# Performance work log

Hardware: AMD Instinct MI355X
Metric: run time of the kernel (lower is better)

The kernel has to match this reference:

```python
import jax, jax.numpy as jnp
import numpy as np

NUM_LAYERS = 2
VOCAB = 32000
IN_FEAT = 256          # embedding dim is IN_FEAT-1, +1 for cue scalar
HIDDEN = 256
ATN = 64               # hardcoded atn_feature_size in GraphConvolution
CLASSES = 2
B, N = 8, 2048


def setup_inputs() -> dict:
    key = jax.random.key(0)
    ks = jax.random.split(key, 12)
    x = jax.random.randint(ks[0], (B, N), 0, VOCAB, dtype=jnp.int32)
    cue = jax.random.randint(ks[1], (B, N), 0, 2, dtype=jnp.int32)
    adj = (jax.random.uniform(ks[2], (B, N, N)) < 0.01).astype(jnp.float32)
    s = 1.0 / np.sqrt(HIDDEN)
    emb_table = jax.random.normal(ks[3], (VOCAB, IN_FEAT - 1), jnp.float32) * 0.02
    Wh = jax.random.uniform(ks[4], (IN_FEAT, HIDDEN), jnp.float32, -s, s)
    bh = jax.random.uniform(ks[5], (HIDDEN,), jnp.float32, -s, s)
    Wq = jax.random.uniform(ks[6], (HIDDEN, ATN), jnp.float32, -s, s)
    Wk = jax.random.uniform(ks[7], (HIDDEN, ATN), jnp.float32, -s, s)
    Wv = jax.random.uniform(ks[8], (HIDDEN, HIDDEN), jnp.float32, -s, s)
    gcb = jax.random.uniform(ks[9], (HIDDEN,), jnp.float32, -s, s)
    Wc = jax.random.uniform(ks[10], (HIDDEN, CLASSES), jnp.float32, -s, s)
    bc = jax.random.uniform(ks[11], (CLASSES,), jnp.float32, -s, s)
    return {"x": x, "cue": cue, "adj": adj, "emb_table": emb_table,
            "Wh": Wh, "bh": bh, "Wq": Wq, "Wk": Wk, "Wv": Wv,
            "gcb": gcb, "Wc": Wc, "bc": bc}


def graph_attention_layer(h, adj, Wq, Wk, Wv, gcb):
    # h: [B,N,H]; adj: [B,N,N] binary. Per node i: softmax over neighbors j of
    # (Wk h_j) . (Wq h_i), weighted sum of Wv h_j. Zero-degree nodes get 0 (pre-bias).
    q = jnp.einsum('bnh,ha->bna', h, Wq)        # [B,N,A]
    k = jnp.einsum('bnh,ha->bna', h, Wk)        # [B,N,A]
    v = jnp.einsum('bnh,hg->bng', h, Wv)        # [B,N,H]
    logits = jnp.einsum('bia,bja->bij', q, k)   # [B,N,N]
    mask = adj > 0
    attn = jax.nn.softmax(jnp.where(mask, logits, -1e9), axis=-1)
    out = jnp.einsum('bij,bjh->bih', attn, v)   # [B,N,H]
    has_nbr = jnp.any(mask, axis=-1, keepdims=True)  # [B,N,1]
    return jnp.where(has_nbr, out, 0.0) + gcb


def reference(x, cue, adj, emb_table, Wh, bh, Wq, Wk, Wv, gcb, Wc, bc):
    emb = emb_table[x]                                   # [B,N,IN_FEAT-1]
    feats = jnp.concatenate([emb, cue.astype(jnp.float32)[..., None]], axis=-1)
    h = jax.nn.relu(jnp.einsum('bnf,fh->bnh', feats, Wh) + bh)
    for _ in range(NUM_LAYERS):
        h = jax.nn.sigmoid(graph_attention_layer(h, adj, Wq, Wk, Wv, gcb))
    logits = jnp.einsum('bnh,hc->bnc', h, Wc) + bc
    return jax.nn.softmax(logits, axis=-1)
```

## Files before the change

### kernel.cpp

```cpp
#include <hip/hip_runtime.h>
#include <hip/hip_bf16.h>


#define NB 8
#define NN 2048
#define ROWS (NB * NN)
#define MAXD 64
#define CSR1 6144

typedef float f4 __attribute__((ext_vector_type(4)));
typedef _Float16 hf;
typedef _Float16 hx2 __attribute__((ext_vector_type(2)));
typedef _Float16 hx4 __attribute__((ext_vector_type(4)));
typedef _Float16 hx8 __attribute__((ext_vector_type(8)));
typedef unsigned int u32;
typedef unsigned short u16;
typedef u16 us8 __attribute__((ext_vector_type(8)));

__device__ __forceinline__ float sigmoidf_(float x) { return 1.f / (1.f + __expf(-x)); }
__device__ __forceinline__ hx2 u2h(u32 u) { union { u32 u; hx2 h; } c; c.u = u; return c.h; }
__device__ __forceinline__ float dot2_(hx2 a, hx2 b, float c) {
#if __has_builtin(__builtin_amdgcn_fdot2)
    return __builtin_amdgcn_fdot2(a, b, c, false);
#else
    return c + (float)a.x * (float)b.x + (float)a.y * (float)b.y;
#endif
}
__device__ __forceinline__ u32 permlo_(u32 hi, u32 lo) { return __builtin_amdgcn_perm(hi, lo, 0x05040100u); }
__device__ __forceinline__ u32 permhi_(u32 hi, u32 lo) { return __builtin_amdgcn_perm(hi, lo, 0x07060302u); }

__device__ __forceinline__ void csr_row(const float* __restrict__ adj,
                                        int* __restrict__ deg, int* __restrict__ nbr,
                                        int row, int t, int* cnt) {
    const f4* ar4 = (const f4*)(adj + (size_t)row * NN);
    if (t == 0) *cnt = 0;
    __syncthreads();
    int* nr = nbr + (size_t)row * MAXD;
#pragma unroll
    for (int it = 0; it < 2; ++it) {
        int idx = it * 256 + t;
        f4 vv = __builtin_nontemporal_load(ar4 + idx);
        if (vv.x > 0.f) { int p = atomicAdd(cnt, 1); if (p < MAXD) nr[p] = idx * 4 + 0; }
        if (vv.y > 0.f) { int p = atomicAdd(cnt, 1); if (p < MAXD) nr[p] = idx * 4 + 1; }
        if (vv.z > 0.f) { int p = atomicAdd(cnt, 1); if (p < MAXD) nr[p] = idx * 4 + 2; }
        if (vv.w > 0.f) { int p = atomicAdd(cnt, 1); if (p < MAXD) nr[p] = idx * 4 + 3; }
    }
    __syncthreads();
    if (t == 0) deg[row] = (*cnt < MAXD) ? *cnt : MAXD;
}

__global__ __launch_bounds__(256) void k_front1(
        const int* __restrict__ x, const int* __restrict__ cue,
        const float* __restrict__ adj, const float* __restrict__ emb,
        const float* __restrict__ Wh, const float* __restrict__ bh,
        const float* __restrict__ Wq, const float* __restrict__ Wk,
        const float* __restrict__ Wv,
        hf* __restrict__ hB, hf* __restrict__ Wpt,
        int* __restrict__ deg, int* __restrict__ nbr) {
    __shared__ float As[32 * 64];
    __shared__ float Ws[32 * 128];
    int bid = blockIdx.x;
    int t = threadIdx.x;

    if (bid < 512) {
        int row0 = (bid >> 1) * 64, col0 = (bid & 1) * 128;
        int srow = t & 63, skg = t >> 6;
        int swc = (t & 31) * 4, swk = t >> 5;
        int tx = t & 15, ty = t >> 4;
        int xr = x[row0 + srow];
        float cv = (float)cue[row0 + srow];
        const float* er = emb + (size_t)xr * 255;

        float acc[4][8];
#pragma unroll
        for (int i = 0; i < 4; ++i)
#pragma unroll
            for (int j = 0; j < 8; ++j) acc[i][j] = 0.f;

        for (int kc = 0; kc < 256; kc += 32) {
            int kb = skg * 8;
#pragma unroll
            for (int u = 0; u < 8; ++u) {
                int f = kc + kb + u;
                As[(kb + u) * 64 + srow] = (f < 255) ? er[f] : cv;
            }
#pragma unroll
            for (int r = 0; r < 4; ++r) {
                int kk = swk + r * 8;
                f4 w = *(const f4*)(Wh + (size_t)(kc + kk) * 256 + col0 + swc);
                *(f4*)&Ws[kk * 128 + swc] = w;
            }
            __syncthreads();
#pragma unroll
            for (int k = 0; k < 32; ++k) {
                f4 av = *(f4*)&As[k * 64 + ty * 4];
                f4 w0 = *(f4*)&Ws[k * 128 + tx * 8];
                f4 w1 = *(f4*)&Ws[k * 128 + tx * 8 + 4];
                float a[4] = {av.x, av.y, av.z, av.w};
                float w[8] = {w0.x, w0.y, w0.z, w0.w, w1.x, w1.y, w1.z, w1.w};
#pragma unroll
                for (int i = 0; i < 4; ++i)
#pragma unroll
                    for (int j = 0; j < 8; ++j) acc[i][j] += a[i] * w[j];
            }
            __syncthreads();
        }
        f4 b0 = *(const f4*)(bh + col0 + tx * 8);
        f4 b1 = *(const f4*)(bh + col0 + tx * 8 + 4);
        float bb[8] = {b0.x, b0.y, b0.z, b0.w, b1.x, b1.y, b1.z, b1.w};
#pragma unroll
        for (int i = 0; i < 4; ++i) {
            int row = row0 + ty * 4 + i;
            hx8 o;
#pragma unroll
            for (int j = 0; j < 8; ++j) o[j] = (hf)fmaxf(acc[i][j] + bb[j], 0.f);
            *(hx8*)(hB + (size_t)row * 256 + col0 + tx * 8) = o;
        }
        return;
    }

    if (bid < 608) {
        int base = (bid - 512) * 256 + t;
#pragma unroll
        for (int r = 0; r < 4; ++r) {
            int i = base + r * 96 * 256;
            int c = i >> 8, f = i & 255;
            float v;
            if (c < 64)       v = Wq[f * 64 + c];
            else if (c < 128) v = Wk[f * 64 + (c - 64)];
            else              v = Wv[f * 256 + (c - 128)];
            Wpt[i] = (hf)v;
        }
        return;
    }

    csr_row(adj, deg, nbr, bid - 608, t, (int*)As);
}

union QSMem {
    struct { u16 As[64 * 40]; u16 Bs[128 * 40]; } q;
    int cnt;
};

__device__ __forceinline__ void qkv_tile(const hf* __restrict__ hB,
                                         const hf* __restrict__ Wpt,
                                         hf* __restrict__ qkvB,
                                         int tile, int t, QSMem& sm) {
    int col0 = (tile % 3) * 128, row0 = (tile / 3) * 64;
    int wave = t >> 6, lane = t & 63;
    int l16 = lane & 15, quad = lane >> 4;
    f4 acc[4][2];
#pragma unroll
    for (int i = 0; i < 4; ++i) { acc[i][0] = (f4){0,0,0,0}; acc[i][1] = (f4){0,0,0,0}; }
    int ar = t >> 2, ao = (t & 3) * 8;
    int bcs = t >> 1, bo = (t & 1) * 16;
    const u16* hB16 = (const u16*)hB;
    const u16* Wp16 = (const u16*)Wpt;

    for (int kc = 0; kc < 256; kc += 32) {
        us8 av  = *(const us8*)(hB16 + (size_t)(row0 + ar) * 256 + kc + ao);
        us8 bv0 = *(const us8*)(Wp16 + (size_t)(col0 + bcs) * 256 + kc + bo);
        us8 bv1 = *(const us8*)(Wp16 + (size_t)(col0 + bcs) * 256 + kc + bo + 8);
        __syncthreads();
        *(us8*)&sm.q.As[ar * 40 + ao] = av;
        *(us8*)&sm.q.Bs[bcs * 40 + bo] = bv0;
        *(us8*)&sm.q.Bs[bcs * 40 + bo + 8] = bv1;
        __syncthreads();
        hx8 afr[4], bfr[2];
#pragma unroll
        for (int mt = 0; mt < 4; ++mt)
            afr[mt] = *(hx8*)&sm.q.As[(mt * 16 + l16) * 40 + quad * 8];
#pragma unroll
        for (int nt = 0; nt < 2; ++nt)
            bfr[nt] = *(hx8*)&sm.q.Bs[((wave * 2 + nt) * 16 + l16) * 40 + quad * 8];
#pragma unroll
        for (int mt = 0; mt < 4; ++mt)
#pragma unroll
            for (int nt = 0; nt < 2; ++nt)
                acc[mt][nt] = __builtin_amdgcn_mfma_f32_16x16x32_f16(
                    afr[mt], bfr[nt], acc[mt][nt], 0, 0, 0);
    }
#pragma unroll
    for (int mt = 0; mt < 4; ++mt)
#pragma unroll
        for (int nt = 0; nt < 2; ++nt) {
            int c = col0 + (wave * 2 + nt) * 16 + l16;
#pragma unroll
            for (int reg = 0; reg < 4; ++reg) {
                int r = row0 + mt * 16 + quad * 4 + reg;
                qkvB[(size_t)r * 384 + c] = (hf)acc[mt][nt][reg];
            }
        }
}

__global__ __launch_bounds__(256) void k_qkv_csr(const hf* __restrict__ hB,
                                                 const hf* __restrict__ Wpt,
                                                 hf* __restrict__ qkvB,
                                                 const float* __restrict__ adj,
                                                 int* __restrict__ deg,
                                                 int* __restrict__ nbr) {
    __shared__ QSMem sm;
    int bid = blockIdx.x, t = threadIdx.x;
    if (bid < 768) qkv_tile(hB, Wpt, qkvB, bid, t, sm);
    else           csr_row(adj, deg, nbr, CSR1 + (bid - 768), t, &sm.cnt);
}

__global__ __launch_bounds__(256) void k_qkv(const hf* __restrict__ hB,
                                             const hf* __restrict__ Wpt,
                                             hf* __restrict__ qkvB) {
    __shared__ QSMem sm;
    qkv_tile(hB, Wpt, qkvB, blockIdx.x, threadIdx.x, sm);
}

template <bool WRITE_OUT>
__global__ __launch_bounds__(256) void k_attn(const hf* __restrict__ qkvB,
                                              const int* __restrict__ deg,
                                              const int* __restrict__ nbr,
                                              const float* __restrict__ gcb,
                                              const float* __restrict__ Wc,
                                              const float* __restrict__ bc,
                                              hf* __restrict__ hB,
                                              float* __restrict__ out) {
    int wave = threadIdx.x >> 6;
    int lane = threadIdx.x & 63;
    int bid = blockIdx.x;
    int row = (bid & 7) * NN + (bid >> 3) * 4 + wave;
    int d = deg[row];
    int l16 = lane & 15, quad = lane >> 4;
    f4 g4 = *(const f4*)(gcb + lane * 4);
    float h0, h1, h2c, h3;
    if (d == 0) {
        h0 = sigmoidf_(g4.x); h1 = sigmoidf_(g4.y);
        h2c = sigmoidf_(g4.z); h3 = sigmoidf_(g4.w);
    } else {
        uint2 qq = *(const uint2*)(qkvB + (size_t)row * 384 + l16 * 4);
        hx2 q01 = u2h(qq.x), q23 = u2h(qq.y);
        int jlane = nbr[(size_t)row * MAXD + lane];
        int bbase = row & ~(NN - 1);
        float m = -1e30f, s = 0.f;
        f4 a = {0, 0, 0, 0};
        for (int e0 = 0; e0 < d; e0 += 16) {
            int jr[4]; uint2 kqr[4]; uint2 vr[4][4];
#pragma unroll
            for (int g = 0; g < 4; ++g) {
                if (e0 + g * 4 < d) {
                    int idx = e0 + g * 4 + quad;
                    jr[g] = __shfl(jlane, idx < d ? idx : 0);
                    kqr[g] = *(const uint2*)(qkvB + (size_t)(bbase + jr[g]) * 384 + 64 + l16 * 4);
                }
            }
#pragma unroll
            for (int g = 0; g < 4; ++g) {
                if (e0 + g * 4 < d) {
                    int j0 = __shfl(jr[g], 0),  j1 = __shfl(jr[g], 16);
                    int j2 = __shfl(jr[g], 32), j3 = __shfl(jr[g], 48);
                    vr[g][0] = *(const uint2*)(qkvB + (size_t)(bbase + j0) * 384 + 128 + lane * 4);
                    vr[g][1] = *(const uint2*)(qkvB + (size_t)(bbase + j1) * 384 + 128 + lane * 4);
                    vr[g][2] = *(const uint2*)(qkvB + (size_t)(bbase + j2) * 384 + 128 + lane * 4);
                    vr[g][3] = *(const uint2*)(qkvB + (size_t)(bbase + j3) * 384 + 128 + lane * 4);
                }
            }
            float pg[4];
#pragma unroll
            for (int g = 0; g < 4; ++g) {
                if (e0 + g * 4 < d) {
                    float p = dot2_(u2h(kqr[g].x), q01, dot2_(u2h(kqr[g].y), q23, 0.f));
                    p += __shfl_xor(p, 1); p += __shfl_xor(p, 2);
                    p += __shfl_xor(p, 4); p += __shfl_xor(p, 8);
                    int idx = e0 + g * 4 + quad;
                    pg[g] = (idx < d) ? p : -1e30f;
                } else pg[g] = -1e30f;
            }
            float cm = fmaxf(fmaxf(pg[0], pg[1]), fmaxf(pg[2], pg[3]));
            cm = fmaxf(cm, __shfl_xor(cm, 16));
            cm = fmaxf(cm, __shfl_xor(cm, 32));
            float mn = fmaxf(m, cm);
            float sc = __expf(m - mn);
            s *= sc; a.x *= sc; a.y *= sc; a.z *= sc; a.w *= sc;
            m = mn;
#pragma unroll
            for (int g = 0; g < 4; ++g) {
                if (e0 + g * 4 < d) {
                    float w = __expf(pg[g] - mn);
                    float sw = w + __shfl_xor(w, 16);
                    sw = sw + __shfl_xor(sw, 32);
                    s += sw;
                    float w0 = __shfl(w, 0),  w1 = __shfl(w, 16);
                    float w2 = __shfl(w, 32), w3 = __shfl(w, 48);
                    hx2 w01, w23;
                    w01.x = (hf)w0; w01.y = (hf)w1;
                    w23.x = (hf)w2; w23.y = (hf)w3;
                    a.x = dot2_(u2h(permlo_(vr[g][1].x, vr[g][0].x)), w01,
                          dot2_(u2h(permlo_(vr[g][3].x, vr[g][2].x)), w23, a.x));
                    a.y = dot2_(u2h(permhi_(vr[g][1].x, vr[g][0].x)), w01,
                          dot2_(u2h(permhi_(vr[g][3].x, vr[g][2].x)), w23, a.y));
                    a.z = dot2_(u2h(permlo_(vr[g][1].y, vr[g][0].y)), w01,
                          dot2_(u2h(permlo_(vr[g][3].y, vr[g][2].y)), w23, a.z));
                    a.w = dot2_(u2h(permhi_(vr[g][1].y, vr[g][0].y)), w01,
                          dot2_(u2h(permhi_(vr[g][3].y, vr[g][2].y)), w23, a.w));
                }
            }
        }
        float inv = 1.f / s;
        h0 = sigmoidf_(a.x * inv + g4.x);
        h1 = sigmoidf_(a.y * inv + g4.y);
        h2c = sigmoidf_(a.z * inv + g4.z);
        h3 = sigmoidf_(a.w * inv + g4.w);
    }
    if (!WRITE_OUT) {
        hx4 o; o.x = (hf)h0; o.y = (hf)h1; o.z = (hf)h2c; o.w = (hf)h3;
        *(hx4*)(hB + (size_t)row * 256 + lane * 4) = o;
    } else {
        f4 wc0 = *(const f4*)(Wc + lane * 8);
        f4 wc1 = *(const f4*)(Wc + lane * 8 + 4);
        float pa = h0 * wc0.x + h1 * wc0.z + h2c * wc1.x + h3 * wc1.z;
        float pb = h0 * wc0.y + h1 * wc0.w + h2c * wc1.y + h3 * wc1.w;
#pragma unroll
        for (int off = 32; off; off >>= 1) {
            pa += __shfl_xor(pa, off);
            pb += __shfl_xor(pb, off);
        }
        if (lane == 0) {
            float l0 = pa + bc[0], l1 = pb + bc[1];
            float mx = fmaxf(l0, l1);
            float e0 = __expf(l0 - mx), e1 = __expf(l1 - mx);
            float inv2 = 1.f / (e0 + e1);
            out[(size_t)row * 2 + 0] = e0 * inv2;
            out[(size_t)row * 2 + 1] = e1 * inv2;
        }
    }
}

extern "C" void kernel_launch(void* const* d_in, const int* in_sizes, int n_in,
                              void* d_out, int out_size, void* d_ws, size_t ws_size,
                              hipStream_t stream) {
    const int*   x    = (const int*)d_in[0];
    const int*   cue  = (const int*)d_in[1];
    const float* adj  = (const float*)d_in[2];
    const float* emb  = (const float*)d_in[3];
    const float* Wh   = (const float*)d_in[4];
    const float* bh   = (const float*)d_in[5];
    const float* Wq   = (const float*)d_in[6];
    const float* Wk   = (const float*)d_in[7];
    const float* Wv   = (const float*)d_in[8];
    const float* gcb  = (const float*)d_in[9];
    const float* Wc   = (const float*)d_in[10];
    const float* bc   = (const float*)d_in[11];
    float* out = (float*)d_out;

    char* w = (char*)d_ws;
    hf*  hB   = (hf*)w;   w += (size_t)ROWS * 256 * 2;
    hf*  qkvB = (hf*)w;   w += (size_t)ROWS * 384 * 2;
    hf*  Wpt  = (hf*)w;   w += (size_t)384 * 256 * 2;
    int* deg  = (int*)w;  w += (size_t)ROWS * 4;
    int* nbr  = (int*)w;

    k_front1<<<608 + CSR1, 256, 0, stream>>>(
        x, cue, adj, emb, Wh, bh, Wq, Wk, Wv, hB, Wpt, deg, nbr);
    k_qkv_csr<<<768 + (ROWS - CSR1), 256, 0, stream>>>(hB, Wpt, qkvB, adj, deg, nbr);
    k_attn<false><<<ROWS / 4, 256, 0, stream>>>(qkvB, deg, nbr, gcb, Wc, bc, hB, out);
    k_qkv<<<768, 256, 0, stream>>>(hB, Wpt, qkvB);
    k_attn<true><<<ROWS / 4, 256, 0, stream>>>(qkvB, deg, nbr, gcb, Wc, bc, hB, out);
}
```

Before: 352.6 us.

## Replace online softmax with two-pass scores-then-weighted-V in attention kernel

The attention kernel now computes all neighbor logits up front, with 4 lanes per neighbor and 16 neighbors per pass over up to MAXD=64, then takes a single wave-wide max/sum softmax and normalizes the weights before the V accumulation. This removes the per-chunk online-softmax rescaling and the final division, and the V gather loop becomes a simple loop over neighbors in groups of 4. The trade-off is that V loads no longer overlap with the K loads and score computation of the same chunk. The code also assumes the degree never exceeds 64.

```diff
diff --git a/kernel.cpp b/kernel.cpp
--- a/kernel.cpp
+++ b/kernel.cpp
@@ -226,86 +226,85 @@
     int bid = blockIdx.x;
     int row = (bid & 7) * NN + (bid >> 3) * 4 + wave;
     int d = deg[row];
-    int l16 = lane & 15, quad = lane >> 4;
     f4 g4 = *(const f4*)(gcb + lane * 4);
     float h0, h1, h2c, h3;
     if (d == 0) {
         h0 = sigmoidf_(g4.x); h1 = sigmoidf_(g4.y);
         h2c = sigmoidf_(g4.z); h3 = sigmoidf_(g4.w);
     } else {
-        uint2 qq = *(const uint2*)(qkvB + (size_t)row * 384 + l16 * 4);
-        hx2 q01 = u2h(qq.x), q23 = u2h(qq.y);
-        int jlane = nbr[(size_t)row * MAXD + lane];
+        const int* jl = nbr + (size_t)row * MAXD;
         int bbase = row & ~(NN - 1);
-        float m = -1e30f, s = 0.f;
+        int jlane = jl[lane < d ? lane : 0];
+        int sub = lane & 3;
+
+        const uint4* qp = (const uint4*)(qkvB + (size_t)row * 384 + sub * 16);
+        uint4 qa = qp[0], qb = qp[1];
+        float pp[4] = {-1e30f, -1e30f, -1e30f, -1e30f};
+#pragma unroll
+        for (int pi = 0; pi < 4; ++pi) {
+            if (pi * 16 < d) {
+                int e = pi * 16 + (lane >> 2);
+                int j = __shfl(jlane, e < d ? e : 0);
+                float p = -1e30f;
+                if (e < d) {
+                    const uint4* kp = (const uint4*)(qkvB + (size_t)(bbase + j) * 384 + 64 + sub * 16);
+                    uint4 ka = kp[0], kb = kp[1];
+                    p = dot2_(u2h(ka.x), u2h(qa.x),
+                        dot2_(u2h(ka.y), u2h(qa.y),
+                        dot2_(u2h(ka.z), u2h(qa.z),
+                        dot2_(u2h(ka.w), u2h(qa.w),
+                        dot2_(u2h(kb.x), u2h(qb.x),
+                        dot2_(u2h(kb.y), u2h(qb.y),
+                        dot2_(u2h(kb.z), u2h(qb.z),
+                        dot2_(u2h(kb.w), u2h(qb.w), 0.f))))))));
+                }
+                p += __shfl_xor(p, 1);
+                p += __shfl_xor(p, 2);
+                pp[pi] = p;
+            }
+        }
+        int src = (lane & 15) << 2;
+        float t0 = __shfl(pp[0], src), t1 = __shfl(pp[1], src);
+        float t2 = __shfl(pp[2], src), t3 = __shfl(pp[3], src);
+        int hi = lane >> 4;
+        float pe = hi == 0 ? t0 : hi == 1 ? t1 : hi == 2 ? t2 : t3;
+        if (lane >= d) pe = -1e30f;
+
+        float mx = pe;
+#pragma unroll
+        for (int off = 32; off; off >>= 1) mx = fmaxf(mx, __shfl_xor(mx, off));
+        float wv = __expf(pe - mx);
+        float sv = wv;
+#pragma unroll
+        for (int off = 32; off; off >>= 1) sv += __shfl_xor(sv, off);
+        float wn = wv * (1.f / sv);
+
         f4 a = {0, 0, 0, 0};
-        for (int e0 = 0; e0 < d; e0 += 16) {
-            int jr[4]; uint2 kqr[4]; uint2 vr[4][4];
-#pragma unroll
-            for (int g = 0; g < 4; ++g) {
-                if (e0 + g * 4 < d) {
-                    int idx = e0 + g * 4 + quad;
-                    jr[g] = __shfl(jlane, idx < d ? idx : 0);
-                    kqr[g] = *(const uint2*)(qkvB + (size_t)(bbase + jr[g]) * 384 + 64 + l16 * 4);
-                }
-            }
-#pragma unroll
-            for (int g = 0; g < 4; ++g) {
-                if (e0 + g * 4 < d) {
-                    int j0 = __shfl(jr[g], 0),  j1 = __shfl(jr[g], 16);
-                    int j2 = __shfl(jr[g], 32), j3 = __shfl(jr[g], 48);
-                    vr[g][0] = *(const uint2*)(qkvB + (size_t)(bbase + j0) * 384 + 128 + lane * 4);
-                    vr[g][1] = *(const uint2*)(qkvB + (size_t)(bbase + j1) * 384 + 128 + lane * 4);
-                    vr[g][2] = *(const uint2*)(qkvB + (size_t)(bbase + j2) * 384 + 128 + lane * 4);
-                    vr[g][3] = *(const uint2*)(qkvB + (size_t)(bbase + j3) * 384 + 128 + lane * 4);
-                }
-            }
-            float pg[4];
-#pragma unroll
-            for (int g = 0; g < 4; ++g) {
-                if (e0 + g * 4 < d) {
-                    float p = dot2_(u2h(kqr[g].x), q01, dot2_(u2h(kqr[g].y), q23, 0.f));
-                    p += __shfl_xor(p, 1); p += __shfl_xor(p, 2);
-                    p += __shfl_xor(p, 4); p += __shfl_xor(p, 8);
-                    int idx = e0 + g * 4 + quad;
-                    pg[g] = (idx < d) ? p : -1e30f;
-                } else pg[g] = -1e30f;
-            }
-            float cm = fmaxf(fmaxf(pg[0], pg[1]), fmaxf(pg[2], pg[3]));
-            cm = fmaxf(cm, __shfl_xor(cm, 16));
-            cm = fmaxf(cm, __shfl_xor(cm, 32));
-            float mn = fmaxf(m, cm);
-            float sc = __expf(m - mn);
-            s *= sc; a.x *= sc; a.y *= sc; a.z *= sc; a.w *= sc;
-            m = mn;
-#pragma unroll
-            for (int g = 0; g < 4; ++g) {
-                if (e0 + g * 4 < d) {
-                    float w = __expf(pg[g] - mn);
-                    float sw = w + __shfl_xor(w, 16);
-                    sw = sw + __shfl_xor(sw, 32);
-                    s += sw;
-                    float w0 = __shfl(w, 0),  w1 = __shfl(w, 16);
-                    float w2 = __shfl(w, 32), w3 = __shfl(w, 48);
-                    hx2 w01, w23;
-                    w01.x = (hf)w0; w01.y = (hf)w1;
-                    w23.x = (hf)w2; w23.y = (hf)w3;
-                    a.x = dot2_(u2h(permlo_(vr[g][1].x, vr[g][0].x)), w01,
-                          dot2_(u2h(permlo_(vr[g][3].x, vr[g][2].x)), w23, a.x));
-                    a.y = dot2_(u2h(permhi_(vr[g][1].x, vr[g][0].x)), w01,
-                          dot2_(u2h(permhi_(vr[g][3].x, vr[g][2].x)), w23, a.y));
-                    a.z = dot2_(u2h(permlo_(vr[g][1].y, vr[g][0].y)), w01,
-                          dot2_(u2h(permlo_(vr[g][3].y, vr[g][2].y)), w23, a.z));
-                    a.w = dot2_(u2h(permhi_(vr[g][1].y, vr[g][0].y)), w01,
-                          dot2_(u2h(permhi_(vr[g][3].y, vr[g][2].y)), w23, a.w));
-                }
-            }
-        }
-        float inv = 1.f / s;
-        h0 = sigmoidf_(a.x * inv + g4.x);
-        h1 = sigmoidf_(a.y * inv + g4.y);
-        h2c = sigmoidf_(a.z * inv + g4.z);
-        h3 = sigmoidf_(a.w * inv + g4.w);
+        for (int g = 0; g < d; g += 4) {
+            float w0 = __shfl(wn, g),     w1 = __shfl(wn, g + 1);
+            float w2 = __shfl(wn, g + 2), w3 = __shfl(wn, g + 3);
+            int j0 = __shfl(jlane, g),     j1 = __shfl(jlane, g + 1);
+            int j2 = __shfl(jlane, g + 2), j3 = __shfl(jlane, g + 3);
+            hx2 w01, w23;
+            w01.x = (hf)w0; w01.y = (hf)w1;
+            w23.x = (hf)w2; w23.y = (hf)w3;
+            uint2 v0 = *(const uint2*)(qkvB + (size_t)(bbase + j0) * 384 + 128 + lane * 4);
+            uint2 v1 = *(const uint2*)(qkvB + (size_t)(bbase + j1) * 384 + 128 + lane * 4);
+            uint2 v2 = *(const uint2*)(qkvB + (size_t)(bbase + j2) * 384 + 128 + lane * 4);
+            uint2 v3 = *(const uint2*)(qkvB + (size_t)(bbase + j3) * 384 + 128 + lane * 4);
+            a.x = dot2_(u2h(permlo_(v1.x, v0.x)), w01,
+                  dot2_(u2h(permlo_(v3.x, v2.x)), w23, a.x));
+            a.y = dot2_(u2h(permhi_(v1.x, v0.x)), w01,
+                  dot2_(u2h(permhi_(v3.x, v2.x)), w23, a.y));
+            a.z = dot2_(u2h(permlo_(v1.y, v0.y)), w01,
+                  dot2_(u2h(permlo_(v3.y, v2.y)), w23, a.z));
+            a.w = dot2_(u2h(permhi_(v1.y, v0.y)), w01,
+                  dot2_(u2h(permhi_(v3.y, v2.y)), w23, a.w));
+        }
+        h0 = sigmoidf_(a.x + g4.x);
+        h1 = sigmoidf_(a.y + g4.y);
+        h2c = sigmoidf_(a.z + g4.z);
+        h3 = sigmoidf_(a.w + g4.w);
     }
     if (!WRITE_OUT) {
         hx4 o; o.x = (hf)h0; o.y = (hf)h1; o.z = (hf)h2c; o.w = (hf)h3;
@@ -322,8 +321,8 @@
         }
         if (lane == 0) {
             float l0 = pa + bc[0], l1 = pb + bc[1];
-            float mx = fmaxf(l0, l1);
-            float e0 = __expf(l0 - mx), e1 = __expf(l1 - mx);
+            float m2 = fmaxf(l0, l1);
+            float e0 = __expf(l0 - m2), e1 = __expf(l1 - m2);
             float inv2 = 1.f / (e0 + e1);
             out[(size_t)row * 2 + 0] = e0 * inv2;
             out[(size_t)row * 2 + 1] = e1 * inv2;
```

New measurement: 342.2 us. -2.9%, faster.
